# Optimization experiments

Hardware: AMD Instinct MI355X
Metric: run time of the kernel (lower is better)

## Reference

```python
import jax, jax.numpy as jnp
import numpy as np

B, S, H, DH = 8, 2048, 4, 32
D = H * DH  # all_head_size = true_hidden_size = 128


def setup_inputs() -> dict:
    key = jax.random.key(0)
    ks = jax.random.split(key, 9)
    inp = {
        "query_tensor": jax.random.normal(ks[0], (B, S, D), dtype=jnp.float32),
        "key_tensor": jax.random.normal(ks[1], (B, S, D), dtype=jnp.float32),
        "value_tensor": jax.random.normal(ks[2], (B, S, D), dtype=jnp.float32),
        "attention_mask": jnp.zeros((B, 1, 1, S), dtype=jnp.float32),
        "head_mask": jnp.ones((1, H, 1, 1), dtype=jnp.float32),
        "Wq": jax.random.normal(ks[3], (D, D), dtype=jnp.float32) * 0.02,
        "bq": jnp.zeros((D,), dtype=jnp.float32),
        "Wk": jax.random.normal(ks[4], (D, D), dtype=jnp.float32) * 0.02,
        "bk": jnp.zeros((D,), dtype=jnp.float32),
        "Wv": jax.random.normal(ks[5], (D, D), dtype=jnp.float32) * 0.02,
        "bv": jnp.zeros((D,), dtype=jnp.float32),
    }
    return inp


def _split_heads(x):
    # (B, S, D) -> (B, H, S, DH)
    return x.reshape(B, S, H, DH).transpose(0, 2, 1, 3)


def reference(query_tensor, key_tensor, value_tensor, attention_mask, head_mask,
              Wq, bq, Wk, bk, Wv, bv):
    q = _split_heads(query_tensor @ Wq + bq)   # (B,H,S,DH)
    k = _split_heads(key_tensor @ Wk + bk)
    v = _split_heads(value_tensor @ Wv + bv)

    scale = 1.0 / jnp.sqrt(jnp.float32(DH))
    scores = jnp.einsum("bhqd,bhkd->bhqk", q, k) * scale + attention_mask
    probs = jax.nn.softmax(scores, axis=-1)
    # dropout is identity at inference (training=False)
    probs = probs * head_mask
    ctx = jnp.einsum("bhqk,bhkd->bhqd", probs, v)  # (B,H,S,DH)
    ctx = ctx.transpose(0, 2, 1, 3).reshape(B, S, D)
    return ctx
```

## Files before the change

kernel.cpp:

```cpp
#include <hip/hip_runtime.h>
#include <hip/hip_bf16.h>
#include <math.h>

#define B_ 8
#define S_ 2048
#define H_ 4
#define DH_ 32
#define D_ 128
#define BS_ (B_ * S_)
#define LOG2E 1.4426950408889634f
#define QSCALE (0.17677669529663687f * LOG2E)

typedef float f32x4  __attribute__((ext_vector_type(4)));
typedef float f32x16 __attribute__((ext_vector_type(16)));
typedef short s16x8  __attribute__((ext_vector_type(8)));

__device__ __forceinline__ unsigned short bf(float x) {
    return __builtin_bit_cast(unsigned short, __float2bfloat16(x));
}
__device__ __forceinline__ float bf2f(unsigned short u) {
    return __builtin_bit_cast(float, (unsigned int)u << 16);
}
__device__ __forceinline__ unsigned int pk2(float a, float b) {
    unsigned int r;
    asm("v_cvt_pk_bf16_f32 %0, %1, %2" : "=v"(r) : "v"(a), "v"(b));
    return r;
}
__device__ __forceinline__ void pswap(unsigned int& a, unsigned int& b) {
    asm volatile("v_permlane32_swap_b32 %0, %1" : "+v"(a), "+v"(b));
}
__device__ __forceinline__ void gll16(const void* g, void* l) {
    __builtin_amdgcn_global_load_lds(
        (const __attribute__((address_space(1))) unsigned int*)(g),
        (__attribute__((address_space(3))) unsigned int*)(l), 16, 0, 0);
}

#define OFF_Q  0u
#define OFF_K  2097152u
#define OFF_V  4194304u
#define OFF_W  6291456u
#define OFF_E  6389760u

__global__ __launch_bounds__(256) void wprep(
    const float* __restrict__ Wq, const float* __restrict__ Wk, const float* __restrict__ Wv,
    const float* __restrict__ maskg,
    unsigned short* __restrict__ Wt, unsigned short* __restrict__ Em)
{
    if (blockIdx.z == 3) {
        const int id16 = blockIdx.y * 4 + blockIdx.x;
        const int base = id16 * 1024 + threadIdx.x * 4;
        float4 m4 = *(const float4*)&maskg[base];
        ushort4 o;
        o.x = bf(__builtin_amdgcn_exp2f(m4.x * LOG2E));
        o.y = bf(__builtin_amdgcn_exp2f(m4.y * LOG2E));
        o.z = bf(__builtin_amdgcn_exp2f(m4.z * LOG2E));
        o.w = bf(__builtin_amdgcn_exp2f(m4.w * LOG2E));
        *(ushort4*)&Em[base] = o;
        return;
    }
    const float* W = (blockIdx.z == 0) ? Wq : (blockIdx.z == 1) ? Wk : Wv;
    unsigned short* Oh = Wt + (size_t)blockIdx.z * D_ * D_;
    unsigned short* Ol = Oh + 3 * D_ * D_;
    __shared__ float tf[32][36];
    const int t = threadIdx.x;
    const int kt = blockIdx.x * 32, ct = blockIdx.y * 32;
    {
        int kl = t >> 3, cl = (t & 7) * 4;
        float4 w4 = *(const float4*)&W[(size_t)(kt + kl) * D_ + ct + cl];
        tf[kl][cl + 0] = w4.x; tf[kl][cl + 1] = w4.y;
        tf[kl][cl + 2] = w4.z; tf[kl][cl + 3] = w4.w;
    }
    __syncthreads();
    {
        int cl = t >> 3, kl = (t & 7) * 4;
        ushort4 oh, ol;
        float v;
        v = tf[kl + 0][cl]; oh.x = bf(v); ol.x = bf(v - bf2f(oh.x));
        v = tf[kl + 1][cl]; oh.y = bf(v); ol.y = bf(v - bf2f(oh.y));
        v = tf[kl + 2][cl]; oh.z = bf(v); ol.z = bf(v - bf2f(oh.z));
        v = tf[kl + 3][cl]; oh.w = bf(v); ol.w = bf(v - bf2f(oh.w));
        *(ushort4*)&Oh[(size_t)(ct + cl) * D_ + kt + kl] = oh;
        *(ushort4*)&Ol[(size_t)(ct + cl) * D_ + kt + kl] = ol;
    }
}

__global__ __launch_bounds__(256) void qkv_mfma(
    const float* __restrict__ Xq, const float* __restrict__ Xk, const float* __restrict__ Xv,
    const unsigned short* __restrict__ Wt, const float* __restrict__ maskg,
    const float* __restrict__ bq, const float* __restrict__ bk, const float* __restrict__ bv,
    unsigned short* __restrict__ Qo, unsigned short* __restrict__ Kf,
    unsigned short* __restrict__ Vf)
{
    const int mode = blockIdx.z, chalf = blockIdx.y;
    const float* X; const float* bias; float scl;
    if (mode == 0)      { X = Xq; bias = bq; scl = QSCALE; }
    else if (mode == 1) { X = Xk; bias = bk; scl = 1.f; }
    else                { X = Xv; bias = bv; scl = 1.f; }
    const unsigned short* WmH = Wt + (size_t)mode * D_ * D_;
    const unsigned short* WmL = WmH + 3 * D_ * D_;

    __shared__ __align__(16) unsigned short xa[2 * 32 * 136];
    __shared__ __align__(16) unsigned short wt[2 * 64 * 136];

    const int t = threadIdx.x;
    const int w = t >> 6, lane = t & 63, lo = lane & 15, hi = lane >> 4;
    const int mf = w >> 1, nb = (w & 1) * 2;

    #pragma unroll
    for (int j = 0; j < 8; j++) {
        int idx = t + 256 * j;
        int part = idx >> 10, i2 = idx & 1023;
        int r = i2 >> 4, c16 = i2 & 15;
        const unsigned short* src = part ? WmL : WmH;
        uint4 v = *(const uint4*)&src[(size_t)(chalf * 64 + r) * D_ + c16 * 8];
        *(uint4*)&wt[part * 8704 + r * 136 + c16 * 8] = v;
    }

    for (int rt = 0; rt < 4; rt++) {
        const long row0 = ((long)blockIdx.x * 4 + rt) * 32;

        __syncthreads();
        #pragma unroll
        for (int j = 0; j < 4; j++) {
            int idx = t + 256 * j;
            int r = idx >> 5, c4 = idx & 31;
            float4 v = *(const float4*)(X + (row0 + r) * D_ + c4 * 4);
            ushort4 ph, pl;
            ph.x = bf(v.x); pl.x = bf(v.x - bf2f(ph.x));
            ph.y = bf(v.y); pl.y = bf(v.y - bf2f(ph.y));
            ph.z = bf(v.z); pl.z = bf(v.z - bf2f(ph.z));
            ph.w = bf(v.w); pl.w = bf(v.w - bf2f(ph.w));
            *(ushort4*)&xa[r * 136 + c4 * 4] = ph;
            *(ushort4*)&xa[4352 + r * 136 + c4 * 4] = pl;
        }
        __syncthreads();

        f32x4 acc[2] = {};
        #pragma unroll
        for (int kk = 0; kk < 4; kk++) {
            const int ko = kk * 32 + hi * 8;
            s16x8 ah = *(const s16x8*)&xa[(mf * 16 + lo) * 136 + ko];
            s16x8 al = *(const s16x8*)&xa[4352 + (mf * 16 + lo) * 136 + ko];
            #pragma unroll
            for (int n2 = 0; n2 < 2; n2++) {
                const int nf = nb + n2;
                s16x8 bh2 = *(const s16x8*)&wt[(nf * 16 + lo) * 136 + ko];
                s16x8 bl2 = *(const s16x8*)&wt[8704 + (nf * 16 + lo) * 136 + ko];
                acc[n2] = __builtin_amdgcn_mfma_f32_16x16x32_bf16(ah, bh2, acc[n2], 0, 0, 0);
                acc[n2] = __builtin_amdgcn_mfma_f32_16x16x32_bf16(al, bh2, acc[n2], 0, 0, 0);
                acc[n2] = __builtin_amdgcn_mfma_f32_16x16x32_bf16(ah, bl2, acc[n2], 0, 0, 0);
            }
        }
        __syncthreads();

        const long b_i = row0 >> 11;
        const long s0g = row0 & 2047;

        if (mode < 2) {
            #pragma unroll
            for (int n2 = 0; n2 < 2; n2++) {
                int c_l = (nb + n2) * 16 + lo;
                float bb = bias[chalf * 64 + c_l];
                #pragma unroll
                for (int r = 0; r < 4; r++) {
                    int s = mf * 16 + hi * 4 + r;
                    xa[s * 72 + c_l] = bf((acc[n2][r] + bb) * scl);
                }
            }
            __syncthreads();
            int s = t >> 3, part = t & 7;
            int c_g = chalf * 64 + part * 8;
            int h = c_g >> 5, dd = c_g & 31;
            long s_i = s0g + s;
            int bh = (int)(b_i * H_ + h);
            uint4 val = *(const uint4*)&xa[s * 72 + part * 8];
            if (mode == 0) {
                *(uint4*)(Qo + ((size_t)bh * S_ + s_i) * DH_ + dd) = val;
            } else {
                int fr = dd >> 4, hwd = (dd >> 3) & 1;
                size_t off = ((((size_t)bh * 64 + (s_i >> 5)) * 2 + fr) * 64
                              + (s_i & 31) + hwd * 32) * 8;
                *(uint4*)(Kf + off) = val;
            }
        } else {
            float emr[4];
            #pragma unroll
            for (int r = 0; r < 4; r++) {
                const int s_l = mf * 16 + hi * 4 + r;
                emr[r] = __builtin_amdgcn_exp2f(maskg[b_i * S_ + s0g + s_l] * LOG2E);
            }
            #pragma unroll
            for (int n2 = 0; n2 < 2; n2++) {
                int c_l = (nb + n2) * 16 + lo;
                float bb = bias[chalf * 64 + c_l];
                #pragma unroll
                for (int r = 0; r < 4; r++) {
                    int s = mf * 16 + hi * 4 + r;
                    xa[c_l * 68 + s] = bf((acc[n2][r] + bb) * emr[r]);
                }
            }
            __syncthreads();
            if (t < 128) {
                int c_l = t >> 1, sh2 = (t & 1) * 16;
                int c_g = chalf * 64 + c_l;
                int h = c_g >> 5, dd = c_g & 31;
                long key0 = s0g + sh2;
                int bh = (int)(b_i * H_ + h);
                size_t base = (((size_t)bh * 128 + (key0 >> 4)) * 64 + dd) * 8;
                uint2 p0 = *(const uint2*)&xa[c_l * 68 + sh2 + 0];
                uint2 p1 = *(const uint2*)&xa[c_l * 68 + sh2 + 4];
                uint2 p2 = *(const uint2*)&xa[c_l * 68 + sh2 + 8];
                uint2 p3 = *(const uint2*)&xa[c_l * 68 + sh2 + 12];
                *(uint4*)(Vf + base)       = make_uint4(p0.x, p0.y, p1.x, p1.y);
                *(uint4*)(Vf + base + 256) = make_uint4(p2.x, p2.y, p3.x, p3.y);
            }
        }
    }
}

__global__ __launch_bounds__(512) void flash_mfma(
    const unsigned short* __restrict__ Qg, const unsigned short* __restrict__ Kfg,
    const unsigned short* __restrict__ Vfg, const unsigned short* __restrict__ Emg,
    const float* __restrict__ head_mask, float* __restrict__ Out)
{
    __shared__ __align__(16) unsigned short smem[18432];

    const int t = threadIdx.x, w = t >> 6, lane = t & 63;
    const int l31 = lane & 31, hw = lane >> 5;
    const int kq = w & 3, qh = w >> 2;

    const int lid = blockIdx.x;
    const int xcd = lid & 7, ser = lid >> 3;
    const int bh = xcd * 4 + (ser >> 5);
    const int qi = ser & 31;
    const int b = bh >> 2, h = bh & 3;
    const int q0 = qi * 64 + qh * 32;

    *(uint2*)&smem[16384 + t * 4] = *(const uint2*)(Emg + (size_t)b * S_ + t * 4);

    const unsigned short* qp = Qg + ((size_t)bh * S_ + q0 + l31) * DH_ + hw * 8;
    const s16x8 qf0 = *(const s16x8*)qp;
    const s16x8 qf1 = *(const s16x8*)(qp + 16);

    const size_t kvbase = (size_t)bh * 65536;
    const unsigned short* ksrc = Kfg + kvbase + (size_t)w * 512 + (size_t)lane * 8;
    const unsigned short* vsrc = Vfg + kvbase + (size_t)w * 512 + (size_t)lane * 8;

    #pragma unroll
    for (int p = 0; p < 2; p++) {
        gll16(ksrc + (size_t)p * 4096, &smem[p * 4096 + w * 512]);
        gll16(vsrc + (size_t)p * 4096, &smem[8192 + p * 4096 + w * 512]);
    }
    __syncthreads();

    const unsigned short* emb = &smem[16384];
    f32x16 ctx = {}, lacc = {};
    const f32x16 z16 = {};

    s16x8 vf_cur0, vf_cur1, ef_cur0, ef_cur1;
    f32x16 s_cur;
    {
        const unsigned short* kb = &smem[kq * 1024];
        const unsigned short* vb = &smem[8192 + kq * 1024];
        s16x8 k0 = *(const s16x8*)(kb + (size_t)lane * 8);
        s16x8 k1 = *(const s16x8*)(kb + 512 + (size_t)lane * 8);
        vf_cur0 = *(const s16x8*)(vb + (size_t)lane * 8);
        vf_cur1 = *(const s16x8*)(vb + 512 + (size_t)lane * 8);
        ef_cur0 = *(const s16x8*)(emb + kq * 32 + hw * 8);
        ef_cur1 = *(const s16x8*)(emb + kq * 32 + hw * 8 + 16);
        s_cur = __builtin_amdgcn_mfma_f32_32x32x16_bf16(k0, qf0, z16, 0, 0, 0);
        s_cur = __builtin_amdgcn_mfma_f32_32x32x16_bf16(k1, qf1, s_cur, 0, 0, 0);
    }

    #pragma unroll
    for (int tile = 0; tile < 16; tile++) {
        asm volatile("s_waitcnt vmcnt(0)" ::: "memory");
        __builtin_amdgcn_sched_barrier(0);
        __builtin_amdgcn_s_barrier();
        __builtin_amdgcn_sched_barrier(0);

        if (tile <= 13) {
            gll16(ksrc + (size_t)(tile + 2) * 4096, &smem[(tile % 2) * 4096 + w * 512]);
            gll16(vsrc + (size_t)(tile + 2) * 4096, &smem[8192 + (tile % 2) * 4096 + w * 512]);
        }

        f32x16 s_next;
        s16x8 vf_n0, vf_n1, ef_n0, ef_n1;
        if (tile < 15) {
            const int nb2 = ((tile + 1) % 2) * 4096 + kq * 1024;
            const unsigned short* kb = &smem[nb2];
            const unsigned short* vb = &smem[8192 + nb2];
            s16x8 kn0 = *(const s16x8*)(kb + (size_t)lane * 8);
            s16x8 kn1 = *(const s16x8*)(kb + 512 + (size_t)lane * 8);
            vf_n0 = *(const s16x8*)(vb + (size_t)lane * 8);
            vf_n1 = *(const s16x8*)(vb + 512 + (size_t)lane * 8);
            ef_n0 = *(const s16x8*)(emb + (tile + 1) * 128 + kq * 32 + hw * 8);
            ef_n1 = *(const s16x8*)(emb + (tile + 1) * 128 + kq * 32 + hw * 8 + 16);
            s_next = __builtin_amdgcn_mfma_f32_32x32x16_bf16(kn0, qf0, z16, 0, 0, 0);
            s_next = __builtin_amdgcn_mfma_f32_32x32x16_bf16(kn1, qf1, s_next, 0, 0, 0);
        }

        unsigned int pd[8];
        #pragma unroll
        for (int j = 0; j < 8; j++) {
            pd[j] = pk2(__builtin_amdgcn_exp2f(s_cur[2 * j]),
                        __builtin_amdgcn_exp2f(s_cur[2 * j + 1]));
        }
        pswap(pd[0], pd[2]); pswap(pd[1], pd[3]);
        pswap(pd[4], pd[6]); pswap(pd[5], pd[7]);
        const s16x8 pa0 = __builtin_bit_cast(s16x8, make_uint4(pd[0], pd[1], pd[2], pd[3]));
        const s16x8 pa1 = __builtin_bit_cast(s16x8, make_uint4(pd[4], pd[5], pd[6], pd[7]));

        ctx  = __builtin_amdgcn_mfma_f32_32x32x16_bf16(pa0, vf_cur0, ctx, 0, 0, 0);
        lacc = __builtin_amdgcn_mfma_f32_32x32x16_bf16(pa0, ef_cur0, lacc, 0, 0, 0);
        ctx  = __builtin_amdgcn_mfma_f32_32x32x16_bf16(pa1, vf_cur1, ctx, 0, 0, 0);
        lacc = __builtin_amdgcn_mfma_f32_32x32x16_bf16(pa1, ef_cur1, lacc, 0, 0, 0);

        if (tile < 15) {
            s_cur = s_next;
            vf_cur0 = vf_n0; vf_cur1 = vf_n1;
            ef_cur0 = ef_n0; ef_cur1 = ef_n1;
        }
    }

    __syncthreads();
    float* ms = (float*)smem;
    #define MS(qh_, sl_, ln_, r_) ms[(((qh_) * 2 + (sl_)) * 64 + (ln_)) * 33 + (r_)]

    if (kq >= 2) {
        #pragma unroll
        for (int r = 0; r < 16; r++) {
            MS(qh, kq - 2, lane, r) = ctx[r];
            MS(qh, kq - 2, lane, 16 + r) = lacc[r];
        }
    }
    __syncthreads();
    if (kq < 2) {
        #pragma unroll
        for (int r = 0; r < 16; r++) {
            ctx[r]  += MS(qh, kq, lane, r);
            lacc[r] += MS(qh, kq, lane, 16 + r);
        }
    }
    __syncthreads();
    if (kq == 1) {
        #pragma unroll
        for (int r = 0; r < 16; r++) {
            MS(qh, 0, lane, r) = ctx[r];
            MS(qh, 0, lane, 16 + r) = lacc[r];
        }
    }
    __syncthreads();
    if (kq == 0) {
        #pragma unroll
        for (int r = 0; r < 16; r++) {
            ctx[r]  += MS(qh, 0, lane, r);
            lacc[r] += MS(qh, 0, lane, 16 + r);
        }
        const float hm = head_mask[h];
        #pragma unroll
        for (int r = 0; r < 16; r++) {
            const int qrow = (r & 3) + 8 * (r >> 2) + 4 * hw;
            Out[((size_t)b * S_ + q0 + qrow) * D_ + h * DH_ + l31] = ctx[r] * hm / lacc[r];
        }
    }
    #undef MS
}

extern "C" void kernel_launch(void* const* d_in, const int* in_sizes, int n_in,
                              void* d_out, int out_size, void* d_ws, size_t ws_size,
                              hipStream_t stream) {
    const float* Xq   = (const float*)d_in[0];
    const float* Xk   = (const float*)d_in[1];
    const float* Xv   = (const float*)d_in[2];
    const float* mask = (const float*)d_in[3];
    const float* hm   = (const float*)d_in[4];
    const float* Wq   = (const float*)d_in[5];
    const float* bq   = (const float*)d_in[6];
    const float* Wk   = (const float*)d_in[7];
    const float* bk   = (const float*)d_in[8];
    const float* Wv   = (const float*)d_in[9];
    const float* bv   = (const float*)d_in[10];
    float* out = (float*)d_out;

    unsigned short* ws = (unsigned short*)d_ws;
    unsigned short* Qo = ws + OFF_Q;
    unsigned short* Kf = ws + OFF_K;
    unsigned short* Vf = ws + OFF_V;
    unsigned short* Wt = ws + OFF_W;
    unsigned short* Em = ws + OFF_E;

    wprep<<<dim3(4, 4, 4), 256, 0, stream>>>(Wq, Wk, Wv, mask, Wt, Em);
    qkv_mfma<<<dim3(128, 2, 3), 256, 0, stream>>>(Xq, Xk, Xv, Wt, mask,
                                                  bq, bk, bv, Qo, Kf, Vf);
    flash_mfma<<<dim3(1024), 512, 0, stream>>>(Qo, Kf, Vf, Em, hm, out);
}
```

Measured before the change: 52.89 us.

## Fuse weight and mask preprocessing into consumer kernels, dropping the wprep launch

Removes the separate wprep kernel. Each qkv_mfma block now transposes and splits its 64-column weight slice into bf16 hi/lo parts directly in LDS, and flash_mfma computes exp(mask) itself when staging it in shared memory. The qkv grid is halved so each block handles 8 row tiles instead of 4, which spreads the redundant per-block weight conversion over more work. Barrier placement moves from the start to the end of each row-tile iteration. The aim is to save a kernel launch and its serialization, at the cost of repeated weight conversion and exp work in every block and fewer qkv blocks in flight.

New measurement: 56.58 us. 1.07x slower.

```diff
diff --git a/kernel.cpp b/kernel.cpp
--- a/kernel.cpp
+++ b/kernel.cpp
@@ -38,66 +38,20 @@
 #define OFF_Q  0u
 #define OFF_K  2097152u
 #define OFF_V  4194304u
-#define OFF_W  6291456u
-#define OFF_E  6389760u
-
-__global__ __launch_bounds__(256) void wprep(
+
+__global__ __launch_bounds__(256) void qkv_mfma(
+    const float* __restrict__ Xq, const float* __restrict__ Xk, const float* __restrict__ Xv,
     const float* __restrict__ Wq, const float* __restrict__ Wk, const float* __restrict__ Wv,
     const float* __restrict__ maskg,
-    unsigned short* __restrict__ Wt, unsigned short* __restrict__ Em)
-{
-    if (blockIdx.z == 3) {
-        const int id16 = blockIdx.y * 4 + blockIdx.x;
-        const int base = id16 * 1024 + threadIdx.x * 4;
-        float4 m4 = *(const float4*)&maskg[base];
-        ushort4 o;
-        o.x = bf(__builtin_amdgcn_exp2f(m4.x * LOG2E));
-        o.y = bf(__builtin_amdgcn_exp2f(m4.y * LOG2E));
-        o.z = bf(__builtin_amdgcn_exp2f(m4.z * LOG2E));
-        o.w = bf(__builtin_amdgcn_exp2f(m4.w * LOG2E));
-        *(ushort4*)&Em[base] = o;
-        return;
-    }
-    const float* W = (blockIdx.z == 0) ? Wq : (blockIdx.z == 1) ? Wk : Wv;
-    unsigned short* Oh = Wt + (size_t)blockIdx.z * D_ * D_;
-    unsigned short* Ol = Oh + 3 * D_ * D_;
-    __shared__ float tf[32][36];
-    const int t = threadIdx.x;
-    const int kt = blockIdx.x * 32, ct = blockIdx.y * 32;
-    {
-        int kl = t >> 3, cl = (t & 7) * 4;
-        float4 w4 = *(const float4*)&W[(size_t)(kt + kl) * D_ + ct + cl];
-        tf[kl][cl + 0] = w4.x; tf[kl][cl + 1] = w4.y;
-        tf[kl][cl + 2] = w4.z; tf[kl][cl + 3] = w4.w;
-    }
-    __syncthreads();
-    {
-        int cl = t >> 3, kl = (t & 7) * 4;
-        ushort4 oh, ol;
-        float v;
-        v = tf[kl + 0][cl]; oh.x = bf(v); ol.x = bf(v - bf2f(oh.x));
-        v = tf[kl + 1][cl]; oh.y = bf(v); ol.y = bf(v - bf2f(oh.y));
-        v = tf[kl + 2][cl]; oh.z = bf(v); ol.z = bf(v - bf2f(oh.z));
-        v = tf[kl + 3][cl]; oh.w = bf(v); ol.w = bf(v - bf2f(oh.w));
-        *(ushort4*)&Oh[(size_t)(ct + cl) * D_ + kt + kl] = oh;
-        *(ushort4*)&Ol[(size_t)(ct + cl) * D_ + kt + kl] = ol;
-    }
-}
-
-__global__ __launch_bounds__(256) void qkv_mfma(
-    const float* __restrict__ Xq, const float* __restrict__ Xk, const float* __restrict__ Xv,
-    const unsigned short* __restrict__ Wt, const float* __restrict__ maskg,
     const float* __restrict__ bq, const float* __restrict__ bk, const float* __restrict__ bv,
     unsigned short* __restrict__ Qo, unsigned short* __restrict__ Kf,
     unsigned short* __restrict__ Vf)
 {
     const int mode = blockIdx.z, chalf = blockIdx.y;
-    const float* X; const float* bias; float scl;
-    if (mode == 0)      { X = Xq; bias = bq; scl = QSCALE; }
-    else if (mode == 1) { X = Xk; bias = bk; scl = 1.f; }
-    else                { X = Xv; bias = bv; scl = 1.f; }
-    const unsigned short* WmH = Wt + (size_t)mode * D_ * D_;
-    const unsigned short* WmL = WmH + 3 * D_ * D_;
+    const float* X; const float* Wf; const float* bias; float scl;
+    if (mode == 0)      { X = Xq; Wf = Wq; bias = bq; scl = QSCALE; }
+    else if (mode == 1) { X = Xk; Wf = Wk; bias = bk; scl = 1.f; }
+    else                { X = Xv; Wf = Wv; bias = bv; scl = 1.f; }
 
     __shared__ __align__(16) unsigned short xa[2 * 32 * 136];
     __shared__ __align__(16) unsigned short wt[2 * 64 * 136];
@@ -106,20 +60,42 @@
     const int w = t >> 6, lane = t & 63, lo = lane & 15, hi = lane >> 4;
     const int mf = w >> 1, nb = (w & 1) * 2;
 
-    #pragma unroll
-    for (int j = 0; j < 8; j++) {
-        int idx = t + 256 * j;
-        int part = idx >> 10, i2 = idx & 1023;
-        int r = i2 >> 4, c16 = i2 & 15;
-        const unsigned short* src = part ? WmL : WmH;
-        uint4 v = *(const uint4*)&src[(size_t)(chalf * 64 + r) * D_ + c16 * 8];
-        *(uint4*)&wt[part * 8704 + r * 136 + c16 * 8] = v;
-    }
-
-    for (int rt = 0; rt < 4; rt++) {
-        const long row0 = ((long)blockIdx.x * 4 + rt) * 32;
-
-        __syncthreads();
+    {
+        float* tf = (float*)xa;
+        #pragma unroll
+        for (int kt = 0; kt < 128; kt += 32) {
+            #pragma unroll
+            for (int ct2 = 0; ct2 < 2; ct2++) {
+                {
+                    const int kl = t >> 3, cl4 = (t & 7) * 4;
+                    float4 w4 = *(const float4*)&Wf[(size_t)(kt + kl) * D_
+                                                    + chalf * 64 + ct2 * 32 + cl4];
+                    tf[kl * 36 + cl4 + 0] = w4.x;
+                    tf[kl * 36 + cl4 + 1] = w4.y;
+                    tf[kl * 36 + cl4 + 2] = w4.z;
+                    tf[kl * 36 + cl4 + 3] = w4.w;
+                }
+                __syncthreads();
+                {
+                    const int cl = t >> 3, kl4 = (t & 7) * 4;
+                    ushort4 oh, ol;
+                    float v;
+                    v = tf[(kl4 + 0) * 36 + cl]; oh.x = bf(v); ol.x = bf(v - bf2f(oh.x));
+                    v = tf[(kl4 + 1) * 36 + cl]; oh.y = bf(v); ol.y = bf(v - bf2f(oh.y));
+                    v = tf[(kl4 + 2) * 36 + cl]; oh.z = bf(v); ol.z = bf(v - bf2f(oh.z));
+                    v = tf[(kl4 + 3) * 36 + cl]; oh.w = bf(v); ol.w = bf(v - bf2f(oh.w));
+                    const int r = ct2 * 32 + cl;
+                    *(ushort4*)&wt[r * 136 + kt + kl4] = oh;
+                    *(ushort4*)&wt[8704 + r * 136 + kt + kl4] = ol;
+                }
+                __syncthreads();
+            }
+        }
+    }
+
+    for (int rt = 0; rt < 8; rt++) {
+        const long row0 = ((long)blockIdx.x * 8 + rt) * 32;
+
         #pragma unroll
         for (int j = 0; j < 4; j++) {
             int idx = t + 256 * j;
@@ -182,6 +158,7 @@
                               + (s_i & 31) + hwd * 32) * 8;
                 *(uint4*)(Kf + off) = val;
             }
+            __syncthreads();
         } else {
             float emr[4];
             #pragma unroll
@@ -214,13 +191,14 @@
                 *(uint4*)(Vf + base)       = make_uint4(p0.x, p0.y, p1.x, p1.y);
                 *(uint4*)(Vf + base + 256) = make_uint4(p2.x, p2.y, p3.x, p3.y);
             }
+            __syncthreads();
         }
     }
 }
 
 __global__ __launch_bounds__(512) void flash_mfma(
     const unsigned short* __restrict__ Qg, const unsigned short* __restrict__ Kfg,
-    const unsigned short* __restrict__ Vfg, const unsigned short* __restrict__ Emg,
+    const unsigned short* __restrict__ Vfg, const float* __restrict__ maskg,
     const float* __restrict__ head_mask, float* __restrict__ Out)
 {
     __shared__ __align__(16) unsigned short smem[18432];
@@ -236,7 +214,15 @@
     const int b = bh >> 2, h = bh & 3;
     const int q0 = qi * 64 + qh * 32;
 
-    *(uint2*)&smem[16384 + t * 4] = *(const uint2*)(Emg + (size_t)b * S_ + t * 4);
+    {
+        float4 m4 = *(const float4*)(maskg + (size_t)b * S_ + t * 4);
+        ushort4 o;
+        o.x = bf(__builtin_amdgcn_exp2f(m4.x * LOG2E));
+        o.y = bf(__builtin_amdgcn_exp2f(m4.y * LOG2E));
+        o.z = bf(__builtin_amdgcn_exp2f(m4.z * LOG2E));
+        o.w = bf(__builtin_amdgcn_exp2f(m4.w * LOG2E));
+        *(ushort4*)&smem[16384 + t * 4] = o;
+    }
 
     const unsigned short* qp = Qg + ((size_t)bh * S_ + q0 + l31) * DH_ + hw * 8;
     const s16x8 qf0 = *(const s16x8*)qp;
@@ -387,11 +373,8 @@
     unsigned short* Qo = ws + OFF_Q;
     unsigned short* Kf = ws + OFF_K;
     unsigned short* Vf = ws + OFF_V;
-    unsigned short* Wt = ws + OFF_W;
-    unsigned short* Em = ws + OFF_E;
-
-    wprep<<<dim3(4, 4, 4), 256, 0, stream>>>(Wq, Wk, Wv, mask, Wt, Em);
-    qkv_mfma<<<dim3(128, 2, 3), 256, 0, stream>>>(Xq, Xk, Xv, Wt, mask,
-                                                  bq, bk, bv, Qo, Kf, Vf);
-    flash_mfma<<<dim3(1024), 512, 0, stream>>>(Qo, Kf, Vf, Em, hm, out);
-}
+
+    qkv_mfma<<<dim3(64, 2, 3), 256, 0, stream>>>(Xq, Xk, Xv, Wq, Wk, Wv, mask,
+                                                 bq, bk, bv, Qo, Kf, Vf);
+    flash_mfma<<<dim3(1024), 512, 0, stream>>>(Qo, Kf, Vf, mask, hm, out);
+}
```
